# Kernel optimization log

Measured on AMD Instinct MI355X. Metric: run time of the kernel, lower is better.

## Reference

```python
import jax, jax.numpy as jnp
import numpy as np

B, L, D, NLAYERS, KCONV = 8, 2048, 1024, 3, 4


def setup_inputs() -> dict:
    key = jax.random.key(0)
    ks = jax.random.split(key, 8)
    inp = {
        "x": jax.random.normal(ks[0], (B, L, D), jnp.float32),
        "conv_w": jax.random.normal(ks[1], (NLAYERS, D, KCONV), jnp.float32) * 0.02,
        "conv_b": jnp.zeros((NLAYERS, D), jnp.float32),
        "wr_w": jax.random.normal(ks[2], (NLAYERS, D, D), jnp.float32) * (1.0 / np.sqrt(D)),
        "wr_b": jnp.zeros((NLAYERS, D), jnp.float32),
        "wi_w": jax.random.normal(ks[3], (NLAYERS, D, D), jnp.float32) * (1.0 / np.sqrt(D)),
        "wi_b": jnp.zeros((NLAYERS, D), jnp.float32),
        "log_a": 3.0 + 0.1 * jax.random.normal(ks[4], (NLAYERS, D), jnp.float32),
        "wo_w": jax.random.normal(ks[5], (NLAYERS, D, D), jnp.float32) * (1.0 / np.sqrt(D)),
        "norm_w": jnp.ones((NLAYERS, D), jnp.float32),
        "norm_out_w": jnp.ones((D,), jnp.float32),
    }
    return inp


def _rmsnorm(x, w, eps=1e-6):
    return x * w * jax.lax.rsqrt(jnp.mean(x * x, axis=-1, keepdims=True) + eps)


def _parallel_scan(a, b):
    # h_t = a_t * h_{t-1} + b_t  via log-space prefix scan (h0 = 0)
    a32 = a.astype(jnp.float32)
    b32 = b.astype(jnp.float32)
    log_A = jnp.cumsum(jnp.log(jnp.maximum(a32, 1e-7)), axis=1)
    log_A = jnp.maximum(log_A, -80.0)  # a<=1 so log_A<=0 already
    A = jnp.exp(log_A)
    h = A * jnp.cumsum(b32 * jnp.exp(-log_A), axis=1)
    return h.astype(a.dtype)


def _rglru_layer(x, cw, cb, wrw, wrb, wiw, wib, la, wow, nw):
    # causal depthwise conv1d, kernel 4, left pad 3
    Lx = x.shape[1]
    xp = jnp.pad(x, ((0, 0), (KCONV - 1, 0), (0, 0)))
    x_conv = cb + sum(xp[:, k:k + Lx, :] * cw[:, k] for k in range(KCONV))
    r_t = jax.nn.sigmoid(x_conv @ wrw.T + wrb)
    i_t = jax.nn.sigmoid(x_conv @ wiw.T + wib)
    a_base = jax.nn.sigmoid(la.astype(jnp.float32)).astype(x.dtype)
    a_t = a_base ** (8.0 * r_t)
    b_t = jnp.sqrt(jnp.clip(1.0 - a_t * a_t, 1e-6, None)) * (i_t * x_conv)
    h = _parallel_scan(a_t, b_t)
    return _rmsnorm(h @ wow.T, nw)


def reference(x, conv_w, conv_b, wr_w, wr_b, wi_w, wi_b, log_a, wo_w, norm_w, norm_out_w):
    h = x
    for l in range(NLAYERS):
        h = _rglru_layer(h, conv_w[l], conv_b[l], wr_w[l], wr_b[l],
                         wi_w[l], wi_b[l], log_a[l], wo_w[l], norm_w[l])
    return _rmsnorm(h, norm_out_w)
```

## Files before the change

kernel.cpp:

```cpp
#include <hip/hip_runtime.h>
#include <type_traits>

#define BDIM 8
#define LDIM 2048
#define DDIM 1024
#define NL 3
#define K4 4
#define MDIM (BDIM * LDIM)
#define BK32 32
#define NT32 (DDIM / BK32)

typedef __bf16 bf16x8 __attribute__((ext_vector_type(8)));
typedef __bf16 bf16x4 __attribute__((ext_vector_type(4)));
typedef float f32x4 __attribute__((ext_vector_type(4)));
typedef const __attribute__((address_space(1))) void gvoid_t;
typedef __attribute__((address_space(3))) void svoid_t;

__device__ __forceinline__ void load16(const void* g, void* lds_uniform) {
    __builtin_amdgcn_global_load_lds((gvoid_t*)g, (svoid_t*)lds_uniform, 16, 0, 0);
}

#define SBAR()                                  \
    do {                                        \
        asm volatile("" ::: "memory");          \
        __builtin_amdgcn_s_barrier();           \
        asm volatile("" ::: "memory");          \
    } while (0)
#define WAITV(N) asm volatile("s_waitcnt vmcnt(" #N ")" ::: "memory")

__global__ void cvt_bf16(const float* __restrict__ s, __bf16* __restrict__ d, int n) {
    int i = blockIdx.x * 256 + threadIdx.x;
    if (i < n) d[i] = (__bf16)s[i];
}

__global__ __launch_bounds__(256) void cvt_interleave(const float* __restrict__ wr,
                                                      const float* __restrict__ wi,
                                                      __bf16* __restrict__ w2, int n) {
    int i = blockIdx.x * 256 + threadIdx.x;
    if (i >= n) return;
    int k = i & (DDIM - 1);
    int ld = i >> 10;
    int l = ld >> 10;
    int d = ld & (DDIM - 1);
    size_t base = ((size_t)l * 2 * DDIM + 2 * d) * DDIM + k;
    w2[base] = (__bf16)wr[i];
    w2[base + DDIM] = (__bf16)wi[i];
}

template <typename T>
__global__ __launch_bounds__(256) void conv_kernel(const T* __restrict__ X,
                                                   const float* __restrict__ cw,
                                                   const float* __restrict__ cb,
                                                   __bf16* __restrict__ XC) {
    int idx = blockIdx.x * 256 + threadIdx.x;
    int d = (idx & (DDIM / 4 - 1)) << 2;
    int t = (idx >> 8) & (LDIM - 1);
    int b = idx >> 19;
    float wv[4][4];
    *(float4*)wv[0] = ((const float4*)cw)[d + 0];
    *(float4*)wv[1] = ((const float4*)cw)[d + 1];
    *(float4*)wv[2] = ((const float4*)cw)[d + 2];
    *(float4*)wv[3] = ((const float4*)cw)[d + 3];
    float4 cbv = *(const float4*)(cb + d);
    float acc[4] = {cbv.x, cbv.y, cbv.z, cbv.w};
#pragma unroll
    for (int k = 0; k < K4; k++) {
        int tt = t + k - (K4 - 1);
        if (tt >= 0) {
            size_t off = ((size_t)(b * LDIM + tt) << 10) + d;
            float xv[4];
            if constexpr (std::is_same<T, float>::value) {
                float4 v = *(const float4*)(X + off);
                xv[0] = v.x; xv[1] = v.y; xv[2] = v.z; xv[3] = v.w;
            } else {
                bf16x4 v = *(const bf16x4*)(X + off);
                xv[0] = (float)v.x; xv[1] = (float)v.y; xv[2] = (float)v.z; xv[3] = (float)v.w;
            }
#pragma unroll
            for (int j = 0; j < 4; j++) acc[j] += xv[j] * wv[j][k];
        }
    }
    bf16x4 o;
    o.x = (__bf16)acc[0]; o.y = (__bf16)acc[1]; o.z = (__bf16)acc[2]; o.w = (__bf16)acc[3];
    *(bf16x4*)(XC + ((size_t)(b * LDIM + t) << 10) + d) = o;
}

__global__ __launch_bounds__(512, 2) void gate_gemm(
    const __bf16* __restrict__ A, const __bf16* __restrict__ W2,
    const float* __restrict__ wrb, const float* __restrict__ wib,
    const float* __restrict__ la,
    __bf16* __restrict__ LOGA, __bf16* __restrict__ BB) {
    __shared__ __attribute__((aligned(16))) __bf16 sm[65536];
    int tid = threadIdx.x;
    int wave = tid >> 6, lane = tid & 63;
    int wm = wave >> 2, wn = wave & 3;
    int fr = lane & 15, quad = lane >> 4;

    int nx = gridDim.x;
    int bid = blockIdx.y * nx + blockIdx.x;
    int cpx = (nx * gridDim.y) >> 3;
    int sw = (bid & 7) * cpx + (bid >> 3);
    int bm0 = (sw / nx) * 256;
    int bn0 = (sw % nx) * 256;

    const __bf16* Ag = A + (size_t)bm0 * DDIM;
    const __bf16* Bg = W2 + (size_t)bn0 * DDIM;

    f32x4 acc[8][4];
    f32x4 zero = {0.f, 0.f, 0.f, 0.f};
#pragma unroll
    for (int i = 0; i < 8; i++)
#pragma unroll
        for (int j = 0; j < 4; j++) acc[i][j] = zero;

    int offA[2][4], offB[4];
#pragma unroll
    for (int mh = 0; mh < 2; mh++)
#pragma unroll
        for (int mi = 0; mi < 4; mi++) {
            int row = wm * 128 + (mh * 4 + mi) * 16 + fr;
            offA[mh][mi] = row * 32 + ((quad ^ ((row >> 1) & 3)) << 3);
        }
#pragma unroll
    for (int ni = 0; ni < 4; ni++) {
        int row = wn * 64 + ni * 16 + fr;
        offB[ni] = 8192 + row * 32 + ((quad ^ ((row >> 1) & 3)) << 3);
    }
    int r0 = tid >> 2, g0 = (tid & 3) ^ ((r0 >> 1) & 3);
    int r1 = (512 + tid) >> 2, g1 = ((512 + tid) & 3) ^ ((r1 >> 1) & 3);
    const __bf16* gA0 = Ag + (size_t)r0 * DDIM + g0 * 8;
    const __bf16* gA1 = Ag + (size_t)r1 * DDIM + g1 * 8;
    const __bf16* gB0 = Bg + (size_t)r0 * DDIM + g0 * 8;
    const __bf16* gB1 = Bg + (size_t)r1 * DDIM + g1 * 8;
    int lb0 = wave * 512, lb1 = 4096 + wave * 512;

    auto STAGE = [&](int buf, const __bf16* pA0, const __bf16* pA1,
                     const __bf16* pB0, const __bf16* pB1, int tc) {
        int lo = buf * 16384;
        load16(pA0 + tc * BK32, sm + lo + lb0);
        load16(pA1 + tc * BK32, sm + lo + lb1);
        load16(pB0 + tc * BK32, sm + lo + 8192 + lb0);
        load16(pB1 + tc * BK32, sm + lo + 8192 + lb1);
    };

    STAGE(0, gA0, gA1, gB0, gB1, 0);
    STAGE(1, gA0, gA1, gB0, gB1, 1);
    STAGE(2, gA0, gA1, gB0, gB1, 2);
    for (int t4 = 0; t4 < NT32; t4 += 4) {
        const __bf16* pA0 = gA0 + (t4 + 3) * BK32;
        const __bf16* pA1 = gA1 + (t4 + 3) * BK32;
        const __bf16* pB0 = gB0 + (t4 + 3) * BK32;
        const __bf16* pB1 = gB1 + (t4 + 3) * BK32;
#pragma unroll
        for (int tt = 0; tt < 4; tt++) {
            int t = t4 + tt;
            if (t + 2 < NT32) { WAITV(8); }
            else if (t + 1 < NT32) { WAITV(4); }
            else { WAITV(0); }
            SBAR();
            if (t + 3 < NT32) STAGE((tt + 3) & 3, pA0, pA1, pB0, pB1, tt);
            const __bf16* base = sm + tt * 16384;
            bf16x8 bfm[4];
#pragma unroll
            for (int ni = 0; ni < 4; ni++) bfm[ni] = *(const bf16x8*)(base + offB[ni]);
#pragma unroll
            for (int mh = 0; mh < 2; mh++) {
                bf16x8 af[4];
#pragma unroll
                for (int mi = 0; mi < 4; mi++)
                    af[mi] = *(const bf16x8*)(base + offA[mh][mi]);
                __builtin_amdgcn_s_setprio(1);
#pragma unroll
                for (int ni = 0; ni < 4; ni++)
#pragma unroll
                    for (int mi = 0; mi < 4; mi++)
                        acc[mh * 4 + mi][ni] = __builtin_amdgcn_mfma_f32_16x16x32_bf16(
                            af[mi], bfm[ni], acc[mh * 4 + mi][ni], 0, 0, 0);
                __builtin_amdgcn_s_setprio(0);
            }
        }
    }

    float* Lt = (float*)&sm[0];
    int colg = (tid & 31) * 8;
    int d0 = (bn0 >> 1) + (colg >> 1);
    float rb[4], ibv[4], lnab[4];
    {
        float4 r4 = *(const float4*)(wrb + d0);
        float4 i4 = *(const float4*)(wib + d0);
        float4 l4 = *(const float4*)(la + d0);
        float lav[4] = {l4.x, l4.y, l4.z, l4.w};
        rb[0] = r4.x; rb[1] = r4.y; rb[2] = r4.z; rb[3] = r4.w;
        ibv[0] = i4.x; ibv[1] = i4.y; ibv[2] = i4.z; ibv[3] = i4.w;
#pragma unroll
        for (int j = 0; j < 4; j++) lnab[j] = __logf(1.f / (1.f + __expf(-lav[j])));
    }
#pragma unroll
    for (int mi = 0; mi < 8; mi++) {
        __syncthreads();
#pragma unroll
        for (int ni = 0; ni < 4; ni++) {
            int col = wn * 64 + ni * 16 + fr;
#pragma unroll
            for (int reg = 0; reg < 4; reg++)
                Lt[(wm * 16 + quad * 4 + reg) * 260 + col] = acc[mi][ni][reg];
        }
        __syncthreads();
#pragma unroll
        for (int hf = 0; hf < 2; hf++) {
            int r = (tid >> 5) + hf * 16;
            int m = bm0 + (r >> 4) * 128 + mi * 16 + (r & 15);
            float vv[8];
            *(f32x4*)&vv[0] = *(const f32x4*)&Lt[r * 260 + colg];
            *(f32x4*)&vv[4] = *(const f32x4*)&Lt[r * 260 + colg + 4];
            bf16x4 xcv = *(const bf16x4*)(A + (size_t)m * DDIM + d0);
            bf16x4 og, ob;
#pragma unroll
            for (int j = 0; j < 4; j++) {
                float rv = 1.f / (1.f + __expf(-(vv[2 * j] + rb[j])));
                float iv = 1.f / (1.f + __expf(-(vv[2 * j + 1] + ibv[j])));
                float lga = 8.f * rv * lnab[j];
                float a = __expf(lga);
                float bt = sqrtf(fmaxf(1.f - a * a, 1e-6f)) * (iv * (float)xcv[j]);
                og[j] = (__bf16)lga;
                ob[j] = (__bf16)bt;
            }
            *(bf16x4*)(LOGA + (size_t)m * DDIM + d0) = og;
            *(bf16x4*)(BB + (size_t)m * DDIM + d0) = ob;
        }
    }
}

__global__ __launch_bounds__(512, 2) void out_gemm(
    const __bf16* __restrict__ A, const __bf16* __restrict__ Wo, __bf16* __restrict__ HW) {
    __shared__ __attribute__((aligned(16))) __bf16 sm[65536];
    int tid = threadIdx.x;
    int wave = tid >> 6, lane = tid & 63;
    int wm = wave >> 2, wn = wave & 3;
    int fr = lane & 15, quad = lane >> 4;

    int nx = gridDim.x;
    int bid = blockIdx.y * nx + blockIdx.x;
    int cpx = (nx * gridDim.y) >> 3;
    int sw = (bid & 7) * cpx + (bid >> 3);
    int bm0 = (sw / nx) * 256;
    int bn0 = (sw % nx) * 256;

    const __bf16* Ag = A + (size_t)bm0 * DDIM;
    const __bf16* Bg = Wo + (size_t)bn0 * DDIM;

    f32x4 acc[8][4];
    f32x4 zero = {0.f, 0.f, 0.f, 0.f};
#pragma unroll
    for (int i = 0; i < 8; i++)
#pragma unroll
        for (int j = 0; j < 4; j++) acc[i][j] = zero;

    int offA[2][4], offB[4];
#pragma unroll
    for (int mh = 0; mh < 2; mh++)
#pragma unroll
        for (int mi = 0; mi < 4; mi++) {
            int row = wm * 128 + (mh * 4 + mi) * 16 + fr;
            offA[mh][mi] = row * 32 + ((quad ^ ((row >> 1) & 3)) << 3);
        }
#pragma unroll
    for (int ni = 0; ni < 4; ni++) {
        int row = wn * 64 + ni * 16 + fr;
        offB[ni] = 8192 + row * 32 + ((quad ^ ((row >> 1) & 3)) << 3);
    }
    int r0 = tid >> 2, g0 = (tid & 3) ^ ((r0 >> 1) & 3);
    int r1 = (512 + tid) >> 2, g1 = ((512 + tid) & 3) ^ ((r1 >> 1) & 3);
    const __bf16* gA0 = Ag + (size_t)r0 * DDIM + g0 * 8;
    const __bf16* gA1 = Ag + (size_t)r1 * DDIM + g1 * 8;
    const __bf16* gB0 = Bg + (size_t)r0 * DDIM + g0 * 8;
    const __bf16* gB1 = Bg + (size_t)r1 * DDIM + g1 * 8;
    int lb0 = wave * 512, lb1 = 4096 + wave * 512;

    auto STAGE = [&](int buf, const __bf16* pA0, const __bf16* pA1,
                     const __bf16* pB0, const __bf16* pB1, int tc) {
        int lo = buf * 16384;
        load16(pA0 + tc * BK32, sm + lo + lb0);
        load16(pA1 + tc * BK32, sm + lo + lb1);
        load16(pB0 + tc * BK32, sm + lo + 8192 + lb0);
        load16(pB1 + tc * BK32, sm + lo + 8192 + lb1);
    };

    STAGE(0, gA0, gA1, gB0, gB1, 0);
    STAGE(1, gA0, gA1, gB0, gB1, 1);
    STAGE(2, gA0, gA1, gB0, gB1, 2);
    for (int t4 = 0; t4 < NT32; t4 += 4) {
        const __bf16* pA0 = gA0 + (t4 + 3) * BK32;
        const __bf16* pA1 = gA1 + (t4 + 3) * BK32;
        const __bf16* pB0 = gB0 + (t4 + 3) * BK32;
        const __bf16* pB1 = gB1 + (t4 + 3) * BK32;
#pragma unroll
        for (int tt = 0; tt < 4; tt++) {
            int t = t4 + tt;
            if (t + 2 < NT32) { WAITV(8); }
            else if (t + 1 < NT32) { WAITV(4); }
            else { WAITV(0); }
            SBAR();
            if (t + 3 < NT32) STAGE((tt + 3) & 3, pA0, pA1, pB0, pB1, tt);
            const __bf16* base = sm + tt * 16384;
            bf16x8 bfm[4];
#pragma unroll
            for (int ni = 0; ni < 4; ni++) bfm[ni] = *(const bf16x8*)(base + offB[ni]);
#pragma unroll
            for (int mh = 0; mh < 2; mh++) {
                bf16x8 af[4];
#pragma unroll
                for (int mi = 0; mi < 4; mi++)
                    af[mi] = *(const bf16x8*)(base + offA[mh][mi]);
                __builtin_amdgcn_s_setprio(1);
#pragma unroll
                for (int ni = 0; ni < 4; ni++)
#pragma unroll
                    for (int mi = 0; mi < 4; mi++)
                        acc[mh * 4 + mi][ni] = __builtin_amdgcn_mfma_f32_16x16x32_bf16(
                            af[mi], bfm[ni], acc[mh * 4 + mi][ni], 0, 0, 0);
                __builtin_amdgcn_s_setprio(0);
            }
        }
    }

    float* Lt = (float*)&sm[0];
    int colg = (tid & 31) * 8;
    int n0 = bn0 + colg;
#pragma unroll
    for (int mi = 0; mi < 8; mi++) {
        __syncthreads();
#pragma unroll
        for (int ni = 0; ni < 4; ni++) {
            int col = wn * 64 + ni * 16 + fr;
#pragma unroll
            for (int reg = 0; reg < 4; reg++)
                Lt[(wm * 16 + quad * 4 + reg) * 260 + col] = acc[mi][ni][reg];
        }
        __syncthreads();
#pragma unroll
        for (int hf = 0; hf < 2; hf++) {
            int r = (tid >> 5) + hf * 16;
            int m = bm0 + (r >> 4) * 128 + mi * 16 + (r & 15);
            float vv[8];
            *(f32x4*)&vv[0] = *(const f32x4*)&Lt[r * 260 + colg];
            *(f32x4*)&vv[4] = *(const f32x4*)&Lt[r * 260 + colg + 4];
            bf16x8 o;
#pragma unroll
            for (int j = 0; j < 8; j++) o[j] = (__bf16)vv[j];
            *(bf16x8*)(HW + (size_t)m * DDIM + n0) = o;
        }
    }
}

#define SCH 32
#define SCT 64
__global__ __launch_bounds__(1024) void scan_kernel(const __bf16* __restrict__ LOGA,
                                                    const __bf16* __restrict__ BB,
                                                    __bf16* __restrict__ H) {
    int b = blockIdx.y;
    int dl = threadIdx.x & 31;
    int d = blockIdx.x * 32 + dl;
    int c = threadIdx.x >> 5;
    size_t base = ((size_t)b * LDIM + (size_t)c * SCT) * DDIM + d;
    const __bf16* pga = LOGA + base;
    const __bf16* pbb = BB + base;
    __bf16* pH = H + base;

    float S = 0.f;
#pragma unroll 8
    for (int t = 0; t < SCT; t++) S += (float)pga[(size_t)t * DDIM];
    __shared__ float sS[SCH][32];
    sS[c][dl] = S;
    __syncthreads();
    float L0 = 0.f;
    for (int cc = 0; cc < c; cc++) L0 += sS[cc][dl];

    float Lr = L0, lcp = fmaxf(L0, -80.f), hB = 0.f;
#pragma unroll 4
    for (int t = 0; t < SCT; t++) {
        float lga = (float)pga[(size_t)t * DDIM];
        Lr += lga;
        float lc = fmaxf(Lr, -80.f);
        hB = __expf(lc - lcp) * hB + (float)pbb[(size_t)t * DDIM];
        lcp = lc;
    }
    float Ac = __expf(fmaxf(Lr, -80.f) - fmaxf(L0, -80.f));
    __shared__ float sA[SCH][32], sB[SCH][32];
    sA[c][dl] = Ac;
    sB[c][dl] = hB;
    __syncthreads();
    float hin = 0.f;
    for (int cc = 0; cc < c; cc++) hin = sA[cc][dl] * hin + sB[cc][dl];

    Lr = L0;
    lcp = fmaxf(L0, -80.f);
    float h = hin;
#pragma unroll 4
    for (int t = 0; t < SCT; t++) {
        float lga = (float)pga[(size_t)t * DDIM];
        Lr += lga;
        float lc = fmaxf(Lr, -80.f);
        h = __expf(lc - lcp) * h + (float)pbb[(size_t)t * DDIM];
        lcp = lc;
        pH[(size_t)t * DDIM] = (__bf16)h;
    }
}

template <typename TI, typename TO>
__global__ __launch_bounds__(256) void rmsnorm_kernel(const TI* __restrict__ X,
                                                      const float* __restrict__ w,
                                                      TO* __restrict__ Y) {
    int row = blockIdx.x;
    int tid = threadIdx.x;
    size_t off = (size_t)row * DDIM + tid * 4;
    float v[4];
    if constexpr (std::is_same<TI, float>::value) {
        float4 t = *(const float4*)(X + off);
        v[0] = t.x; v[1] = t.y; v[2] = t.z; v[3] = t.w;
    } else {
        bf16x4 t = *(const bf16x4*)(X + off);
        v[0] = (float)t.x; v[1] = (float)t.y; v[2] = (float)t.z; v[3] = (float)t.w;
    }
    float s = v[0] * v[0] + v[1] * v[1] + v[2] * v[2] + v[3] * v[3];
#pragma unroll
    for (int o = 32; o > 0; o >>= 1) s += __shfl_down(s, o);
    __shared__ float sw[4];
    if ((tid & 63) == 0) sw[tid >> 6] = s;
    __syncthreads();
    float tot = sw[0] + sw[1] + sw[2] + sw[3];
    float scale = rsqrtf(tot * (1.f / (float)DDIM) + 1e-6f);
    float4 wv = ((const float4*)w)[tid];
    float o0 = v[0] * wv.x * scale, o1 = v[1] * wv.y * scale;
    float o2 = v[2] * wv.z * scale, o3 = v[3] * wv.w * scale;
    if constexpr (std::is_same<TO, float>::value) {
        float4 o = {o0, o1, o2, o3};
        *(float4*)(Y + off) = o;
    } else {
        bf16x4 o;
        o.x = (__bf16)o0; o.y = (__bf16)o1; o.z = (__bf16)o2; o.w = (__bf16)o3;
        *(bf16x4*)(Y + off) = o;
    }
}

extern "C" void kernel_launch(void* const* d_in, const int* in_sizes, int n_in,
                              void* d_out, int out_size, void* d_ws, size_t ws_size,
                              hipStream_t stream) {
    const float* x = (const float*)d_in[0];
    const float* conv_w = (const float*)d_in[1];
    const float* conv_b = (const float*)d_in[2];
    const float* wr_w = (const float*)d_in[3];
    const float* wr_b = (const float*)d_in[4];
    const float* wi_w = (const float*)d_in[5];
    const float* wi_b = (const float*)d_in[6];
    const float* log_a = (const float*)d_in[7];
    const float* wo_w = (const float*)d_in[8];
    const float* norm_w = (const float*)d_in[9];
    const float* norm_out_w = (const float*)d_in[10];

    const size_t W2SZ = (size_t)NL * 2 * DDIM * DDIM;
    const size_t WOSZ = (size_t)NL * DDIM * DDIM;
    const size_t MD = (size_t)MDIM * DDIM;
    __bf16* w2 = (__bf16*)d_ws;
    __bf16* wo16 = w2 + W2SZ;
    __bf16* XC = wo16 + WOSZ;
    __bf16* LGA = XC + MD;
    __bf16* BBf = LGA + MD;
    __bf16* Hb = BBf + MD;
    __bf16* HWb = Hb + MD;
    __bf16* PNb = HWb + MD;

    int nw = (int)WOSZ;
    cvt_interleave<<<(nw + 255) / 256, 256, 0, stream>>>(wr_w, wi_w, w2, nw);
    cvt_bf16<<<(nw + 255) / 256, 256, 0, stream>>>(wo_w, wo16, nw);

    for (int l = 0; l < NL; l++) {
        if (l == 0)
            conv_kernel<float><<<(MDIM * (DDIM / 4)) / 256, 256, 0, stream>>>(
                x, conv_w, conv_b, XC);
        else
            conv_kernel<__bf16><<<(MDIM * (DDIM / 4)) / 256, 256, 0, stream>>>(
                PNb, conv_w + (size_t)l * DDIM * K4, conv_b + (size_t)l * DDIM, XC);
        gate_gemm<<<dim3(2 * DDIM / 256, MDIM / 256), 512, 0, stream>>>(
            XC, w2 + (size_t)l * 2 * DDIM * DDIM,
            wr_b + (size_t)l * DDIM, wi_b + (size_t)l * DDIM, log_a + (size_t)l * DDIM,
            LGA, BBf);
        scan_kernel<<<dim3(DDIM / 32, BDIM), 1024, 0, stream>>>(LGA, BBf, Hb);
        out_gemm<<<dim3(DDIM / 256, MDIM / 256), 512, 0, stream>>>(
            Hb, wo16 + (size_t)l * DDIM * DDIM, HWb);
        rmsnorm_kernel<__bf16, __bf16><<<MDIM, 256, 0, stream>>>(
            HWb, norm_w + (size_t)l * DDIM, PNb);
    }
    rmsnorm_kernel<__bf16, float><<<MDIM, 256, 0, stream>>>(PNb, norm_out_w, (float*)d_out);
}
```

Baseline: 911.4 us.

## Pre-swizzle weights into MFMA fragment order and load B directly to registers

Weight conversion kernels now write bf16 weights in a per-lane MFMA fragment layout. Both GEMMs then load B operands straight from global memory into registers, with one step of prefetch, instead of staging them through LDS. Only A is staged in LDS, now triple-buffered in 48KB instead of 128KB. This cuts LDS traffic and footprint per block, but B fetches depend on L2 hits and software prefetch to hide global latency, and the wait counts are hand-tuned.

```diff
diff --git a/kernel.cpp b/kernel.cpp
--- a/kernel.cpp
+++ b/kernel.cpp
@@ -28,23 +28,28 @@
     } while (0)
 #define WAITV(N) asm volatile("s_waitcnt vmcnt(" #N ")" ::: "memory")
 
-__global__ void cvt_bf16(const float* __restrict__ s, __bf16* __restrict__ d, int n) {
-    int i = blockIdx.x * 256 + threadIdx.x;
-    if (i < n) d[i] = (__bf16)s[i];
-}
-
-__global__ __launch_bounds__(256) void cvt_interleave(const float* __restrict__ wr,
-                                                      const float* __restrict__ wi,
-                                                      __bf16* __restrict__ w2, int n) {
-    int i = blockIdx.x * 256 + threadIdx.x;
-    if (i >= n) return;
-    int k = i & (DDIM - 1);
-    int ld = i >> 10;
-    int l = ld >> 10;
-    int d = ld & (DDIM - 1);
-    size_t base = ((size_t)l * 2 * DDIM + 2 * d) * DDIM + k;
-    w2[base] = (__bf16)wr[i];
-    w2[base + DDIM] = (__bf16)wi[i];
+template <bool ILV>
+__global__ __launch_bounds__(256) void cvt_frag(const float* __restrict__ s0,
+                                                const float* __restrict__ s1,
+                                                __bf16* __restrict__ dst, int per_layer) {
+    int c = blockIdx.x * 256 + threadIdx.x;
+    int l = c / per_layer, cc = c - l * per_layer;
+    int lane = cc & 63;
+    int sub = (cc >> 6) & 15;
+    int t = (cc >> 10) & 31;
+    int pan = cc >> 15;
+    int n = pan * 256 + ((sub >> 2) << 6) + ((sub & 3) << 4) + (lane & 15);
+    int k = (t << 5) + ((lane >> 4) << 3);
+    const float* src;
+    if constexpr (ILV) {
+        src = ((n & 1) ? s1 : s0) + (size_t)l * DDIM * DDIM + (size_t)(n >> 1) * DDIM + k;
+    } else {
+        src = s0 + (size_t)l * DDIM * DDIM + (size_t)n * DDIM + k;
+    }
+    bf16x8 o;
+#pragma unroll
+    for (int j = 0; j < 8; j++) o[j] = (__bf16)src[j];
+    *(bf16x8*)(dst + (size_t)c * 8) = o;
 }
 
 template <typename T>
@@ -86,11 +91,11 @@
 }
 
 __global__ __launch_bounds__(512, 2) void gate_gemm(
-    const __bf16* __restrict__ A, const __bf16* __restrict__ W2,
+    const __bf16* __restrict__ A, const __bf16* __restrict__ WF,
     const float* __restrict__ wrb, const float* __restrict__ wib,
     const float* __restrict__ la,
     __bf16* __restrict__ LOGA, __bf16* __restrict__ BB) {
-    __shared__ __attribute__((aligned(16))) __bf16 sm[65536];
+    __shared__ __attribute__((aligned(16))) __bf16 sm[3 * 8192];
     int tid = threadIdx.x;
     int wave = tid >> 6, lane = tid & 63;
     int wm = wave >> 2, wn = wave & 3;
@@ -101,10 +106,11 @@
     int cpx = (nx * gridDim.y) >> 3;
     int sw = (bid & 7) * cpx + (bid >> 3);
     int bm0 = (sw / nx) * 256;
-    int bn0 = (sw % nx) * 256;
+    int pan = sw % nx;
+    int bn0 = pan * 256;
 
     const __bf16* Ag = A + (size_t)bm0 * DDIM;
-    const __bf16* Bg = W2 + (size_t)bn0 * DDIM;
+    const __bf16* bw = WF + ((size_t)pan * (NT32 * 16) + wn * 4) * 512 + lane * 8;
 
     f32x4 acc[8][4];
     f32x4 zero = {0.f, 0.f, 0.f, 0.f};
@@ -113,7 +119,7 @@
 #pragma unroll
         for (int j = 0; j < 4; j++) acc[i][j] = zero;
 
-    int offA[2][4], offB[4];
+    int offA[2][4];
 #pragma unroll
     for (int mh = 0; mh < 2; mh++)
 #pragma unroll
@@ -121,64 +127,67 @@
             int row = wm * 128 + (mh * 4 + mi) * 16 + fr;
             offA[mh][mi] = row * 32 + ((quad ^ ((row >> 1) & 3)) << 3);
         }
-#pragma unroll
-    for (int ni = 0; ni < 4; ni++) {
-        int row = wn * 64 + ni * 16 + fr;
-        offB[ni] = 8192 + row * 32 + ((quad ^ ((row >> 1) & 3)) << 3);
-    }
     int r0 = tid >> 2, g0 = (tid & 3) ^ ((r0 >> 1) & 3);
     int r1 = (512 + tid) >> 2, g1 = ((512 + tid) & 3) ^ ((r1 >> 1) & 3);
     const __bf16* gA0 = Ag + (size_t)r0 * DDIM + g0 * 8;
     const __bf16* gA1 = Ag + (size_t)r1 * DDIM + g1 * 8;
-    const __bf16* gB0 = Bg + (size_t)r0 * DDIM + g0 * 8;
-    const __bf16* gB1 = Bg + (size_t)r1 * DDIM + g1 * 8;
     int lb0 = wave * 512, lb1 = 4096 + wave * 512;
 
-    auto STAGE = [&](int buf, const __bf16* pA0, const __bf16* pA1,
-                     const __bf16* pB0, const __bf16* pB1, int tc) {
-        int lo = buf * 16384;
-        load16(pA0 + tc * BK32, sm + lo + lb0);
-        load16(pA1 + tc * BK32, sm + lo + lb1);
-        load16(pB0 + tc * BK32, sm + lo + 8192 + lb0);
-        load16(pB1 + tc * BK32, sm + lo + 8192 + lb1);
+    auto STAGE = [&](int buf, int t) {
+        load16(gA0 + t * BK32, sm + buf * 8192 + lb0);
+        load16(gA1 + t * BK32, sm + buf * 8192 + lb1);
     };
-
-    STAGE(0, gA0, gA1, gB0, gB1, 0);
-    STAGE(1, gA0, gA1, gB0, gB1, 1);
-    STAGE(2, gA0, gA1, gB0, gB1, 2);
-    for (int t4 = 0; t4 < NT32; t4 += 4) {
-        const __bf16* pA0 = gA0 + (t4 + 3) * BK32;
-        const __bf16* pA1 = gA1 + (t4 + 3) * BK32;
-        const __bf16* pB0 = gB0 + (t4 + 3) * BK32;
-        const __bf16* pB1 = gB1 + (t4 + 3) * BK32;
-#pragma unroll
-        for (int tt = 0; tt < 4; tt++) {
-            int t = t4 + tt;
-            if (t + 2 < NT32) { WAITV(8); }
-            else if (t + 1 < NT32) { WAITV(4); }
-            else { WAITV(0); }
-            SBAR();
-            if (t + 3 < NT32) STAGE((tt + 3) & 3, pA0, pA1, pB0, pB1, tt);
-            const __bf16* base = sm + tt * 16384;
-            bf16x8 bfm[4];
-#pragma unroll
-            for (int ni = 0; ni < 4; ni++) bfm[ni] = *(const bf16x8*)(base + offB[ni]);
-#pragma unroll
-            for (int mh = 0; mh < 2; mh++) {
-                bf16x8 af[4];
+    auto LOADB = [&](bf16x8* dst, int t) {
+#pragma unroll
+        for (int ni = 0; ni < 4; ni++)
+            dst[ni] = *(const bf16x8*)(bw + (size_t)t * 8192 + ni * 512);
+    };
+    auto COMPUTE = [&](const __bf16* base, const bf16x8* bc) {
+#pragma unroll
+        for (int mh = 0; mh < 2; mh++) {
+            bf16x8 af[4];
+#pragma unroll
+            for (int mi = 0; mi < 4; mi++) af[mi] = *(const bf16x8*)(base + offA[mh][mi]);
+            __builtin_amdgcn_s_setprio(1);
+#pragma unroll
+            for (int ni = 0; ni < 4; ni++)
 #pragma unroll
                 for (int mi = 0; mi < 4; mi++)
-                    af[mi] = *(const bf16x8*)(base + offA[mh][mi]);
-                __builtin_amdgcn_s_setprio(1);
-#pragma unroll
-                for (int ni = 0; ni < 4; ni++)
-#pragma unroll
-                    for (int mi = 0; mi < 4; mi++)
-                        acc[mh * 4 + mi][ni] = __builtin_amdgcn_mfma_f32_16x16x32_bf16(
-                            af[mi], bfm[ni], acc[mh * 4 + mi][ni], 0, 0, 0);
-                __builtin_amdgcn_s_setprio(0);
-            }
-        }
+                    acc[mh * 4 + mi][ni] = __builtin_amdgcn_mfma_f32_16x16x32_bf16(
+                        af[mi], bc[ni], acc[mh * 4 + mi][ni], 0, 0, 0);
+            __builtin_amdgcn_s_setprio(0);
+        }
+    };
+
+    STAGE(0, 0);
+    STAGE(1, 1);
+    bf16x8 bnxt[4];
+    LOADB(bnxt, 0);
+    {
+        WAITV(6); SBAR();
+        STAGE(2, 2);
+        bf16x8 bc[4];
+#pragma unroll
+        for (int ni = 0; ni < 4; ni++) bc[ni] = bnxt[ni];
+        LOADB(bnxt, 1);
+        COMPUTE(sm, bc);
+    }
+    for (int tg = 1; tg <= 28; tg += 3) {
+#pragma unroll
+        for (int u = 0; u < 3; u++) {
+            int t = tg + u;
+            WAITV(10); SBAR();
+            if (t + 2 < NT32) STAGE(u, t + 2);
+            bf16x8 bc[4];
+#pragma unroll
+            for (int ni = 0; ni < 4; ni++) bc[ni] = bnxt[ni];
+            LOADB(bnxt, t + 1);
+            COMPUTE(sm + ((1 + u) % 3) * 8192, bc);
+        }
+    }
+    {
+        WAITV(8); SBAR();
+        COMPUTE(sm + 8192, bnxt);
     }
 
     float* Lt = (float*)&sm[0];
@@ -232,8 +241,8 @@
 }
 
 __global__ __launch_bounds__(512, 2) void out_gemm(
-    const __bf16* __restrict__ A, const __bf16* __restrict__ Wo, __bf16* __restrict__ HW) {
-    __shared__ __attribute__((aligned(16))) __bf16 sm[65536];
+    const __bf16* __restrict__ A, const __bf16* __restrict__ WF, __bf16* __restrict__ HW) {
+    __shared__ __attribute__((aligned(16))) __bf16 sm[3 * 8192];
     int tid = threadIdx.x;
     int wave = tid >> 6, lane = tid & 63;
     int wm = wave >> 2, wn = wave & 3;
@@ -244,10 +253,11 @@
     int cpx = (nx * gridDim.y) >> 3;
     int sw = (bid & 7) * cpx + (bid >> 3);
     int bm0 = (sw / nx) * 256;
-    int bn0 = (sw % nx) * 256;
+    int pan = sw % nx;
+    int bn0 = pan * 256;
 
     const __bf16* Ag = A + (size_t)bm0 * DDIM;
-    const __bf16* Bg = Wo + (size_t)bn0 * DDIM;
+    const __bf16* bw = WF + ((size_t)pan * (NT32 * 16) + wn * 4) * 512 + lane * 8;
 
     f32x4 acc[8][4];
     f32x4 zero = {0.f, 0.f, 0.f, 0.f};
@@ -256,7 +266,7 @@
 #pragma unroll
         for (int j = 0; j < 4; j++) acc[i][j] = zero;
 
-    int offA[2][4], offB[4];
+    int offA[2][4];
 #pragma unroll
     for (int mh = 0; mh < 2; mh++)
 #pragma unroll
@@ -264,64 +274,67 @@
             int row = wm * 128 + (mh * 4 + mi) * 16 + fr;
             offA[mh][mi] = row * 32 + ((quad ^ ((row >> 1) & 3)) << 3);
         }
-#pragma unroll
-    for (int ni = 0; ni < 4; ni++) {
-        int row = wn * 64 + ni * 16 + fr;
-        offB[ni] = 8192 + row * 32 + ((quad ^ ((row >> 1) & 3)) << 3);
-    }
     int r0 = tid >> 2, g0 = (tid & 3) ^ ((r0 >> 1) & 3);
     int r1 = (512 + tid) >> 2, g1 = ((512 + tid) & 3) ^ ((r1 >> 1) & 3);
     const __bf16* gA0 = Ag + (size_t)r0 * DDIM + g0 * 8;
     const __bf16* gA1 = Ag + (size_t)r1 * DDIM + g1 * 8;
-    const __bf16* gB0 = Bg + (size_t)r0 * DDIM + g0 * 8;
-    const __bf16* gB1 = Bg + (size_t)r1 * DDIM + g1 * 8;
     int lb0 = wave * 512, lb1 = 4096 + wave * 512;
 
-    auto STAGE = [&](int buf, const __bf16* pA0, const __bf16* pA1,
-                     const __bf16* pB0, const __bf16* pB1, int tc) {
-        int lo = buf * 16384;
-        load16(pA0 + tc * BK32, sm + lo + lb0);
-        load16(pA1 + tc * BK32, sm + lo + lb1);
-        load16(pB0 + tc * BK32, sm + lo + 8192 + lb0);
-        load16(pB1 + tc * BK32, sm + lo + 8192 + lb1);
+    auto STAGE = [&](int buf, int t) {
+        load16(gA0 + t * BK32, sm + buf * 8192 + lb0);
+        load16(gA1 + t * BK32, sm + buf * 8192 + lb1);
     };
-
-    STAGE(0, gA0, gA1, gB0, gB1, 0);
-    STAGE(1, gA0, gA1, gB0, gB1, 1);
-    STAGE(2, gA0, gA1, gB0, gB1, 2);
-    for (int t4 = 0; t4 < NT32; t4 += 4) {
-        const __bf16* pA0 = gA0 + (t4 + 3) * BK32;
-        const __bf16* pA1 = gA1 + (t4 + 3) * BK32;
-        const __bf16* pB0 = gB0 + (t4 + 3) * BK32;
-        const __bf16* pB1 = gB1 + (t4 + 3) * BK32;
-#pragma unroll
-        for (int tt = 0; tt < 4; tt++) {
-            int t = t4 + tt;
-            if (t + 2 < NT32) { WAITV(8); }
-            else if (t + 1 < NT32) { WAITV(4); }
-            else { WAITV(0); }
-            SBAR();
-            if (t + 3 < NT32) STAGE((tt + 3) & 3, pA0, pA1, pB0, pB1, tt);
-            const __bf16* base = sm + tt * 16384;
-            bf16x8 bfm[4];
-#pragma unroll
-            for (int ni = 0; ni < 4; ni++) bfm[ni] = *(const bf16x8*)(base + offB[ni]);
-#pragma unroll
-            for (int mh = 0; mh < 2; mh++) {
-                bf16x8 af[4];
+    auto LOADB = [&](bf16x8* dst, int t) {
+#pragma unroll
+        for (int ni = 0; ni < 4; ni++)
+            dst[ni] = *(const bf16x8*)(bw + (size_t)t * 8192 + ni * 512);
+    };
+    auto COMPUTE = [&](const __bf16* base, const bf16x8* bc) {
+#pragma unroll
+        for (int mh = 0; mh < 2; mh++) {
+            bf16x8 af[4];
+#pragma unroll
+            for (int mi = 0; mi < 4; mi++) af[mi] = *(const bf16x8*)(base + offA[mh][mi]);
+            __builtin_amdgcn_s_setprio(1);
+#pragma unroll
+            for (int ni = 0; ni < 4; ni++)
 #pragma unroll
                 for (int mi = 0; mi < 4; mi++)
-                    af[mi] = *(const bf16x8*)(base + offA[mh][mi]);
-                __builtin_amdgcn_s_setprio(1);
-#pragma unroll
-                for (int ni = 0; ni < 4; ni++)
-#pragma unroll
-                    for (int mi = 0; mi < 4; mi++)
-                        acc[mh * 4 + mi][ni] = __builtin_amdgcn_mfma_f32_16x16x32_bf16(
-                            af[mi], bfm[ni], acc[mh * 4 + mi][ni], 0, 0, 0);
-                __builtin_amdgcn_s_setprio(0);
-            }
-        }
+                    acc[mh * 4 + mi][ni] = __builtin_amdgcn_mfma_f32_16x16x32_bf16(
+                        af[mi], bc[ni], acc[mh * 4 + mi][ni], 0, 0, 0);
+            __builtin_amdgcn_s_setprio(0);
+        }
+    };
+
+    STAGE(0, 0);
+    STAGE(1, 1);
+    bf16x8 bnxt[4];
+    LOADB(bnxt, 0);
+    {
+        WAITV(6); SBAR();
+        STAGE(2, 2);
+        bf16x8 bc[4];
+#pragma unroll
+        for (int ni = 0; ni < 4; ni++) bc[ni] = bnxt[ni];
+        LOADB(bnxt, 1);
+        COMPUTE(sm, bc);
+    }
+    for (int tg = 1; tg <= 28; tg += 3) {
+#pragma unroll
+        for (int u = 0; u < 3; u++) {
+            int t = tg + u;
+            WAITV(10); SBAR();
+            if (t + 2 < NT32) STAGE(u, t + 2);
+            bf16x8 bc[4];
+#pragma unroll
+            for (int ni = 0; ni < 4; ni++) bc[ni] = bnxt[ni];
+            LOADB(bnxt, t + 1);
+            COMPUTE(sm + ((1 + u) % 3) * 8192, bc);
+        }
+    }
+    {
+        WAITV(8); SBAR();
+        COMPUTE(sm + 8192, bnxt);
     }
 
     float* Lt = (float*)&sm[0];
@@ -461,18 +474,17 @@
     const size_t W2SZ = (size_t)NL * 2 * DDIM * DDIM;
     const size_t WOSZ = (size_t)NL * DDIM * DDIM;
     const size_t MD = (size_t)MDIM * DDIM;
-    __bf16* w2 = (__bf16*)d_ws;
-    __bf16* wo16 = w2 + W2SZ;
-    __bf16* XC = wo16 + WOSZ;
+    __bf16* w2f = (__bf16*)d_ws;
+    __bf16* wof = w2f + W2SZ;
+    __bf16* XC = wof + WOSZ;
     __bf16* LGA = XC + MD;
     __bf16* BBf = LGA + MD;
     __bf16* Hb = BBf + MD;
     __bf16* HWb = Hb + MD;
     __bf16* PNb = HWb + MD;
 
-    int nw = (int)WOSZ;
-    cvt_interleave<<<(nw + 255) / 256, 256, 0, stream>>>(wr_w, wi_w, w2, nw);
-    cvt_bf16<<<(nw + 255) / 256, 256, 0, stream>>>(wo_w, wo16, nw);
+    cvt_frag<true><<<(NL * 262144) / 256, 256, 0, stream>>>(wr_w, wi_w, w2f, 262144);
+    cvt_frag<false><<<(NL * 131072) / 256, 256, 0, stream>>>(wo_w, nullptr, wof, 131072);
 
     for (int l = 0; l < NL; l++) {
         if (l == 0)
@@ -482,12 +494,12 @@
             conv_kernel<__bf16><<<(MDIM * (DDIM / 4)) / 256, 256, 0, stream>>>(
                 PNb, conv_w + (size_t)l * DDIM * K4, conv_b + (size_t)l * DDIM, XC);
         gate_gemm<<<dim3(2 * DDIM / 256, MDIM / 256), 512, 0, stream>>>(
-            XC, w2 + (size_t)l * 2 * DDIM * DDIM,
+            XC, w2f + (size_t)l * 2 * DDIM * DDIM,
             wr_b + (size_t)l * DDIM, wi_b + (size_t)l * DDIM, log_a + (size_t)l * DDIM,
             LGA, BBf);
         scan_kernel<<<dim3(DDIM / 32, BDIM), 1024, 0, stream>>>(LGA, BBf, Hb);
         out_gemm<<<dim3(DDIM / 256, MDIM / 256), 512, 0, stream>>>(
-            Hb, wo16 + (size_t)l * DDIM * DDIM, HWb);
+            Hb, wof + (size_t)l * DDIM * DDIM, HWb);
         rmsnorm_kernel<__bf16, __bf16><<<MDIM, 256, 0, stream>>>(
             HWb, norm_w + (size_t)l * DDIM, PNb);
     }
```

After: 967.7 us. 6.2% more time.
